# Performance work log

Measured on AMD Instinct MI355X. Metric: run time of the kernel, lower is better.

## Reference

```python
import jax, jax.numpy as jnp
import numpy as np

N_PTS = 1_000_000
RES = 512
RANK = 48
OUT = 32
INIT_SCALE = 0.1


def _plane_sample(plane, gx, gy):
    """Bilinear grid_sample, align_corners=True, border padding.
    plane: [R, Res, Res] (R=rank); gx, gy: [N] in [-1,1] -> [R, N]."""
    res = plane.shape[-1]
    px = jnp.clip((gx + 1.0) * 0.5 * (res - 1), 0.0, res - 1.0)
    py = jnp.clip((gy + 1.0) * 0.5 * (res - 1), 0.0, res - 1.0)
    x0 = jnp.floor(px).astype(jnp.int32)
    y0 = jnp.floor(py).astype(jnp.int32)
    x1 = jnp.minimum(x0 + 1, res - 1)
    y1 = jnp.minimum(y0 + 1, res - 1)
    wx = px - x0.astype(px.dtype)
    wy = py - y0.astype(py.dtype)
    # gathers: [R, N] each
    v00 = plane[:, y0, x0]
    v01 = plane[:, y0, x1]
    v10 = plane[:, y1, x0]
    v11 = plane[:, y1, x1]
    return (v00 * (1 - wy) * (1 - wx) + v01 * (1 - wy) * wx
            + v10 * wy * (1 - wx) + v11 * wy * wx)


def _line_sample(line, gy):
    """Line is [R, Res] (width dim of size 1 collapses; x coord is 0 -> px=0).
    1-D linear interp along Res with gy in [-1,1] -> [R, N]."""
    res = line.shape[-1]
    py = jnp.clip((gy + 1.0) * 0.5 * (res - 1), 0.0, res - 1.0)
    y0 = jnp.floor(py).astype(jnp.int32)
    y1 = jnp.minimum(y0 + 1, res - 1)
    wy = py - y0.astype(py.dtype)
    return line[:, y0] * (1 - wy) + line[:, y1] * wy


def _geo_forward(coordinates, plane_xy, plane_xz, plane_yz,
                 line_z, line_y, line_x, proj_w, proj_b):
    coords = coordinates * 2.0 - 1.0  # [N, 3] in [-1, 1]
    cx, cy, cz = coords[:, 0], coords[:, 1], coords[:, 2]
    vm = (_plane_sample(plane_xy, cx, cy) * _line_sample(line_z, cz)
          + _plane_sample(plane_xz, cx, cz) * _line_sample(line_y, cy)
          + _plane_sample(plane_yz, cy, cz) * _line_sample(line_x, cx))  # [R, N]
    # projection: [N, R] @ [R, OUT] + b
    return vm.T @ proj_w.T + proj_b


def setup_inputs() -> dict:
    key = jax.random.key(0)
    ks = jax.random.split(key, 9)
    return {
        "coordinates": jax.random.uniform(ks[0], (N_PTS, 3), dtype=jnp.float32),
        "plane_xy": jax.random.normal(ks[1], (RANK, RES, RES), jnp.float32) * INIT_SCALE,
        "plane_xz": jax.random.normal(ks[2], (RANK, RES, RES), jnp.float32) * INIT_SCALE,
        "plane_yz": jax.random.normal(ks[3], (RANK, RES, RES), jnp.float32) * INIT_SCALE,
        "line_z": jax.random.normal(ks[4], (RANK, RES), jnp.float32) * INIT_SCALE,
        "line_y": jax.random.normal(ks[5], (RANK, RES), jnp.float32) * INIT_SCALE,
        "line_x": jax.random.normal(ks[6], (RANK, RES), jnp.float32) * INIT_SCALE,
        "proj_w": jax.random.normal(ks[7], (OUT, RANK), jnp.float32) * INIT_SCALE,
        "proj_b": jnp.zeros((OUT,), jnp.float32),
    }


def reference(coordinates, plane_xy, plane_xz, plane_yz,
              line_z, line_y, line_x, proj_w, proj_b):
    return _geo_forward(coordinates, plane_xy, plane_xz, plane_yz,
                        line_z, line_y, line_x, proj_w, proj_b)
```

## Files before the change

### kernel.cpp

```cpp
#include <hip/hip_runtime.h>
#include <stdint.h>

#define RES      512
#define TEXELS   (RES * RES)
#define NPTS     1000000
#define RANK     48
#define ODIM     32
#define PPB      64
#define VMS      52
#define OSTR     36
#define TT       128
#define TS       25

typedef unsigned int u32;
typedef float vf4 __attribute__((ext_vector_type(4)));

__device__ __forceinline__ float lobf(u32 u) { return __uint_as_float(u << 16); }
__device__ __forceinline__ float hibf(u32 u) { return __uint_as_float(u & 0xffff0000u); }

__device__ __forceinline__ float ntl(const float* p) {
    return __builtin_nontemporal_load(p);
}

__device__ __forceinline__ u32 pkbf(float a, float b) {
    u32 x = __float_as_uint(a), y = __float_as_uint(b);
    u32 xr = (x + 0x7fffu + ((x >> 16) & 1u)) >> 16;
    u32 yr = (y + 0x7fffu + ((y >> 16) & 1u)) & 0xffff0000u;
    return xr | yr;
}

template <int TEXB>
__global__ __launch_bounds__(256) void transpose_planes(
    const float* __restrict__ p0, const float* __restrict__ p1,
    const float* __restrict__ p2, char* __restrict__ ws)
{
    __shared__ u32 lds[TT * TS + 8];

    int t = threadIdx.x;
    int base = blockIdx.x * TT;
    int plane = blockIdx.y;
    const float* src = (plane == 0) ? p0 : ((plane == 1) ? p1 : p2);

    int t7 = t & (TT - 1);
    int half = t >> 7;
#pragma unroll
    for (int j = 0; j < 12; ++j) {
        int d = half * 12 + j;
        float a = ntl(&src[(size_t)(2 * d) * TEXELS + base + t7]);
        float b = ntl(&src[(size_t)(2 * d + 1) * TEXELS + base + t7]);
        lds[t7 * TS + d] = pkbf(a, b);
    }
    __syncthreads();

    char* outp = ws + (size_t)plane * TEXELS * TEXB + (size_t)base * TEXB;
    constexpr int NS = TT * TEXB / (16 * 256);
#pragma unroll
    for (int s = 0; s < NS; ++s) {
        u32 o = (u32)(s * 256 + t) * 16u;
        u32 texel, rem;
        if (TEXB == 128) { texel = o >> 7; rem = o & 127u; }
        else {
            texel = ((o >> 5) * 43691u) >> 17;
            rem = o - texel * 96u;
        }
        u32 dw = texel * TS + (rem >> 2);
        uint4 q = make_uint4(lds[dw], lds[dw + 1], lds[dw + 2], lds[dw + 3]);
        *(uint4*)(outp + o) = q;
    }
}

template <int TEXB>
__global__ __launch_bounds__(256) void transpose_lines(
    const float* __restrict__ lz, const float* __restrict__ ly,
    const float* __restrict__ lx, char* __restrict__ ws)
{
    int id = blockIdx.x * 256 + threadIdx.x;
    int line = id >> 9;
    int pos = id & (RES - 1);
    const float* src = (line == 0) ? lz : ((line == 1) ? ly : lx);
    char* dst = ws + (size_t)3 * TEXELS * TEXB + (size_t)line * RES * TEXB
                   + (size_t)pos * TEXB;
#pragma unroll
    for (int k = 0; k < 6; ++k) {
        uint4 q;
        q.x = pkbf(ntl(&src[(8 * k + 0) * RES + pos]), ntl(&src[(8 * k + 1) * RES + pos]));
        q.y = pkbf(ntl(&src[(8 * k + 2) * RES + pos]), ntl(&src[(8 * k + 3) * RES + pos]));
        q.z = pkbf(ntl(&src[(8 * k + 4) * RES + pos]), ntl(&src[(8 * k + 5) * RES + pos]));
        q.w = pkbf(ntl(&src[(8 * k + 6) * RES + pos]), ntl(&src[(8 * k + 7) * RES + pos]));
        *(uint4*)(dst + 16 * k) = q;
    }
}

__device__ __forceinline__ void prep1(float g, int& i0, int& i1, float& w) {
    float p = fminf(fmaxf((g + 1.f) * 0.5f * 511.f, 0.f), 511.f);
    float fp = floorf(p);
    i0 = (int)fp;
    i1 = min(i0 + 1, RES - 1);
    w = p - fp;
}

template <int TEXB>
__global__ __launch_bounds__(512, 4) void geo_main(
    const float* __restrict__ coords, const char* __restrict__ ws,
    const float* __restrict__ W, const float* __restrict__ Bb,
    float* __restrict__ out)
{
    __shared__ float vm_lds[PPB * VMS];

    int tid = threadIdx.x;
    int ptL = tid >> 3;
    int c = tid & 7;
    int pt = blockIdx.x * PPB + ptL;

    float gx = ntl(&coords[3 * pt + 0]) * 2.f - 1.f;
    float gy = ntl(&coords[3 * pt + 1]) * 2.f - 1.f;
    float gz = ntl(&coords[3 * pt + 2]) * 2.f - 1.f;

    int x0, x1, y0, y1, z0, z1;
    float wx, wy, wz;
    prep1(gx, x0, x1, wx);
    prep1(gy, y0, y1, wy);
    prep1(gz, z0, z1, wz);

    const size_t PW = (size_t)TEXELS * TEXB;
    const size_t LW = (size_t)RES * TEXB;
    const char* pxy = ws;
    const char* pxz = ws + PW;
    const char* pyz = ws + 2 * PW;
    const char* lzb = ws + 3 * PW;
    const char* lyb = lzb + LW;
    const char* lxb = lyb + LW;

    u32 co = 12u * (u32)c;

    u32 q[12][3], le[3][3], lf[3][3];
    {
        u32 offs[12];
        offs[0] = (u32)(y0 * RES + x0) * TEXB + co;
        offs[1] = (u32)(y0 * RES + x1) * TEXB + co;
        offs[2] = (u32)(y1 * RES + x0) * TEXB + co;
        offs[3] = (u32)(y1 * RES + x1) * TEXB + co;
        offs[4] = (u32)(z0 * RES + x0) * TEXB + co;
        offs[5] = (u32)(z0 * RES + x1) * TEXB + co;
        offs[6] = (u32)(z1 * RES + x0) * TEXB + co;
        offs[7] = (u32)(z1 * RES + x1) * TEXB + co;
        offs[8]  = (u32)(z0 * RES + y0) * TEXB + co;
        offs[9]  = (u32)(z0 * RES + y1) * TEXB + co;
        offs[10] = (u32)(z1 * RES + y0) * TEXB + co;
        offs[11] = (u32)(z1 * RES + y1) * TEXB + co;
        const char* bases[3] = { pxy, pxz, pyz };
#pragma unroll
        for (int p = 0; p < 3; ++p) {
#pragma unroll
            for (int k = 0; k < 4; ++k) {
                const u32* s = (const u32*)(bases[p] + offs[4 * p + k]);
                q[4 * p + k][0] = s[0];
                q[4 * p + k][1] = s[1];
                q[4 * p + k][2] = s[2];
            }
        }
        const char* lb[3] = { lzb, lyb, lxb };
        u32 l0[3] = { (u32)z0 * TEXB + co, (u32)y0 * TEXB + co, (u32)x0 * TEXB + co };
        u32 l1[3] = { (u32)z1 * TEXB + co, (u32)y1 * TEXB + co, (u32)x1 * TEXB + co };
#pragma unroll
        for (int p = 0; p < 3; ++p) {
            const u32* s0 = (const u32*)(lb[p] + l0[p]);
            const u32* s1 = (const u32*)(lb[p] + l1[p]);
            le[p][0] = s0[0]; le[p][1] = s0[1]; le[p][2] = s0[2];
            lf[p][0] = s1[0]; lf[p][1] = s1[1]; lf[p][2] = s1[2];
        }
    }

    float pw[3][4];
    pw[0][0] = (1.f - wy) * (1.f - wx); pw[0][1] = (1.f - wy) * wx;
    pw[0][2] = wy * (1.f - wx);         pw[0][3] = wy * wx;
    pw[1][0] = (1.f - wz) * (1.f - wx); pw[1][1] = (1.f - wz) * wx;
    pw[1][2] = wz * (1.f - wx);         pw[1][3] = wz * wx;
    pw[2][0] = (1.f - wz) * (1.f - wy); pw[2][1] = (1.f - wz) * wy;
    pw[2][2] = wz * (1.f - wy);         pw[2][3] = wz * wy;
    float lw[3] = { wz, wy, wx };

    float vm[6] = { 0.f, 0.f, 0.f, 0.f, 0.f, 0.f };
#pragma unroll
    for (int p = 0; p < 3; ++p) {
        float s0 = pw[p][0], s1 = pw[p][1], s2 = pw[p][2], s3 = pw[p][3];
        float il = 1.f - lw[p], wl = lw[p];
#pragma unroll
        for (int d = 0; d < 3; ++d) {
            u32 a = q[4 * p + 0][d], b = q[4 * p + 1][d];
            u32 cc = q[4 * p + 2][d], dd = q[4 * p + 3][d];
            float slo = s0 * lobf(a) + s1 * lobf(b) + s2 * lobf(cc) + s3 * lobf(dd);
            float shi = s0 * hibf(a) + s1 * hibf(b) + s2 * hibf(cc) + s3 * hibf(dd);
            float llo = il * lobf(le[p][d]) + wl * lobf(lf[p][d]);
            float lhi = il * hibf(le[p][d]) + wl * hibf(lf[p][d]);
            vm[2 * d + 0] = fmaf(slo, llo, vm[2 * d + 0]);
            vm[2 * d + 1] = fmaf(shi, lhi, vm[2 * d + 1]);
        }
    }

    float* vr = vm_lds + ptL * VMS + 6 * c;
    *(float2*)(vr + 0) = make_float2(vm[0], vm[1]);
    *(float2*)(vr + 2) = make_float2(vm[2], vm[3]);
    *(float2*)(vr + 4) = make_float2(vm[4], vm[5]);

    __syncthreads();

    int wav = __builtin_amdgcn_readfirstlane(tid >> 6);
    int lane = tid & 63;
    int ob = wav * 4;

    const float* vmrow = vm_lds + lane * VMS;
    float4 bb = *(const float4*)(Bb + ob);
    float a0 = bb.x, a1 = bb.y, a2 = bb.z, a3 = bb.w;
#pragma unroll 4
    for (int k = 0; k < 12; ++k) {
        float4 v = *(const float4*)(vmrow + 4 * k);
        float4 w0 = *(const float4*)(W + (ob + 0) * RANK + 4 * k);
        float4 w1 = *(const float4*)(W + (ob + 1) * RANK + 4 * k);
        float4 w2 = *(const float4*)(W + (ob + 2) * RANK + 4 * k);
        float4 w3 = *(const float4*)(W + (ob + 3) * RANK + 4 * k);
        a0 = fmaf(v.x, w0.x, a0); a0 = fmaf(v.y, w0.y, a0);
        a0 = fmaf(v.z, w0.z, a0); a0 = fmaf(v.w, w0.w, a0);
        a1 = fmaf(v.x, w1.x, a1); a1 = fmaf(v.y, w1.y, a1);
        a1 = fmaf(v.z, w1.z, a1); a1 = fmaf(v.w, w1.w, a1);
        a2 = fmaf(v.x, w2.x, a2); a2 = fmaf(v.y, w2.y, a2);
        a2 = fmaf(v.z, w2.z, a2); a2 = fmaf(v.w, w2.w, a2);
        a3 = fmaf(v.x, w3.x, a3); a3 = fmaf(v.y, w3.y, a3);
        a3 = fmaf(v.z, w3.z, a3); a3 = fmaf(v.w, w3.w, a3);
    }

    __syncthreads();
    {
        vf4 r; r.x = a0; r.y = a1; r.z = a2; r.w = a3;
        *(vf4*)(vm_lds + lane * OSTR + ob) = r;
    }
    __syncthreads();
    {
        int p8 = lane >> 3;
        int c2 = lane & 7;
        vf4 v = *(const vf4*)(vm_lds + (wav * 8 + p8) * OSTR + 4 * c2);
        size_t o2 = (size_t)(blockIdx.x * PPB + wav * 8 + p8) * ODIM + 4 * c2;
        __builtin_nontemporal_store(v, (vf4*)(out + o2));
    }
}

template <int TEXB>
static void launch_all(const float* coords, const float* pxy, const float* pxz,
                       const float* pyz, const float* lz, const float* ly,
                       const float* lx, const float* W, const float* Bb,
                       float* out, char* ws, hipStream_t stream) {
    dim3 gt(TEXELS / TT, 3);
    transpose_planes<TEXB><<<gt, 256, 0, stream>>>(pxy, pxz, pyz, ws);
    transpose_lines<TEXB><<<6, 256, 0, stream>>>(lz, ly, lx, ws);
    geo_main<TEXB><<<NPTS / PPB, 512, 0, stream>>>(coords, ws, W, Bb, out);
}

extern "C" void kernel_launch(void* const* d_in, const int* in_sizes, int n_in,
                              void* d_out, int out_size, void* d_ws, size_t ws_size,
                              hipStream_t stream) {
    const float* coords = (const float*)d_in[0];
    const float* pxy = (const float*)d_in[1];
    const float* pxz = (const float*)d_in[2];
    const float* pyz = (const float*)d_in[3];
    const float* lz = (const float*)d_in[4];
    const float* ly = (const float*)d_in[5];
    const float* lx = (const float*)d_in[6];
    const float* W = (const float*)d_in[7];
    const float* Bb = (const float*)d_in[8];
    float* out = (float*)d_out;
    char* ws = (char*)d_ws;

    size_t need128 = (size_t)3 * TEXELS * 128 + (size_t)3 * RES * 128;
    if (ws_size >= need128)
        launch_all<128>(coords, pxy, pxz, pyz, lz, ly, lx, W, Bb, out, ws, stream);
    else
        launch_all<96>(coords, pxy, pxz, pyz, lz, ly, lx, W, Bb, out, ws, stream);
}
```

Before: 469.4 us.

## Sort points by Morton cell before sampling to improve gather locality

Adds a counting sort of points into 32^3 Morton-ordered cells (count, scan, scatter kernels) and runs the main sampling kernel on the reordered coordinates, scattering output rows back through a permutation. Block indices are also remapped so that consecutive sorted chunks land on the same XCD. The intent is to make the bilinear texel gathers from the 96-byte-per-texel planes cache-friendly instead of random. The cost is several extra kernel launches, global atomics on clustered cells, and an extra pass over the coordinates. The output LDS stride also changes from 36 to 33.

```diff
diff --git a/kernel.cpp b/kernel.cpp
--- a/kernel.cpp
+++ b/kernel.cpp
@@ -8,9 +8,10 @@
 #define ODIM     32
 #define PPB      64
 #define VMS      52
-#define OSTR     36
+#define OSTR     33
 #define TT       128
 #define TS       25
+#define CELLS    32768
 
 typedef unsigned int u32;
 typedef float vf4 __attribute__((ext_vector_type(4)));
@@ -19,6 +20,9 @@
 __device__ __forceinline__ float hibf(u32 u) { return __uint_as_float(u & 0xffff0000u); }
 
 __device__ __forceinline__ float ntl(const float* p) {
+    return __builtin_nontemporal_load(p);
+}
+__device__ __forceinline__ u32 ntlu(const u32* p) {
     return __builtin_nontemporal_load(p);
 }
 
@@ -27,6 +31,20 @@
     u32 xr = (x + 0x7fffu + ((x >> 16) & 1u)) >> 16;
     u32 yr = (y + 0x7fffu + ((y >> 16) & 1u)) & 0xffff0000u;
     return xr | yr;
+}
+
+__device__ __forceinline__ u32 sprd5(u32 a) {
+    a &= 31u;
+    a = (a | (a << 8)) & 0x100Fu;
+    a = (a | (a << 4)) & 0x10C3u;
+    a = (a | (a << 2)) & 0x1249u;
+    return a;
+}
+__device__ __forceinline__ u32 cellOf(float x, float y, float z) {
+    u32 cx = (u32)fminf(fmaxf(x * 32.f, 0.f), 31.f);
+    u32 cy = (u32)fminf(fmaxf(y * 32.f, 0.f), 31.f);
+    u32 cz = (u32)fminf(fmaxf(z * 32.f, 0.f), 31.f);
+    return sprd5(cx) | (sprd5(cy) << 1) | (sprd5(cz) << 2);
 }
 
 template <int TEXB>
@@ -91,6 +109,71 @@
     }
 }
 
+__global__ __launch_bounds__(256) void zero_counts(u32* __restrict__ counts) {
+    counts[blockIdx.x * 256 + threadIdx.x] = 0u;
+}
+
+__global__ __launch_bounds__(256) void cell_count(
+    const float* __restrict__ coords, u32* __restrict__ counts)
+{
+    int pt = blockIdx.x * 256 + threadIdx.x;
+    if (pt >= NPTS) return;
+    float x = ntl(&coords[3 * pt + 0]);
+    float y = ntl(&coords[3 * pt + 1]);
+    float z = ntl(&coords[3 * pt + 2]);
+    atomicAdd(&counts[cellOf(x, y, z)], 1u);
+}
+
+__global__ __launch_bounds__(1024) void cell_scan(
+    const u32* __restrict__ counts, u32* __restrict__ cursors)
+{
+    __shared__ u32 wt[16];
+    int t = threadIdx.x;
+    u32 local[32];
+    u32 s = 0;
+#pragma unroll
+    for (int i = 0; i < 32; ++i) {
+        local[i] = s;
+        s += counts[t * 32 + i];
+    }
+    u32 tot = s;
+    int lane = t & 63, w = t >> 6;
+    u32 incl = tot;
+#pragma unroll
+    for (int d = 1; d < 64; d <<= 1) {
+        u32 v = __shfl_up(incl, d);
+        if (lane >= d) incl += v;
+    }
+    if (lane == 63) wt[w] = incl;
+    __syncthreads();
+    if (t == 0) {
+        u32 a = 0;
+#pragma unroll
+        for (int i = 0; i < 16; ++i) { u32 x = wt[i]; wt[i] = a; a += x; }
+    }
+    __syncthreads();
+    u32 base = wt[w] + (incl - tot);
+#pragma unroll
+    for (int i = 0; i < 32; ++i)
+        cursors[t * 32 + i] = base + local[i];
+}
+
+__global__ __launch_bounds__(256) void cell_scatter(
+    const float* __restrict__ coords, u32* __restrict__ cursors,
+    u32* __restrict__ perm, float* __restrict__ rc)
+{
+    int pt = blockIdx.x * 256 + threadIdx.x;
+    if (pt >= NPTS) return;
+    float x = ntl(&coords[3 * pt + 0]);
+    float y = ntl(&coords[3 * pt + 1]);
+    float z = ntl(&coords[3 * pt + 2]);
+    u32 pos = atomicAdd(&cursors[cellOf(x, y, z)], 1u);
+    perm[pos] = (u32)pt;
+    rc[3 * pos + 0] = x;
+    rc[3 * pos + 1] = y;
+    rc[3 * pos + 2] = z;
+}
+
 __device__ __forceinline__ void prep1(float g, int& i0, int& i1, float& w) {
     float p = fminf(fmaxf((g + 1.f) * 0.5f * 511.f, 0.f), 511.f);
     float fp = floorf(p);
@@ -99,22 +182,35 @@
     w = p - fp;
 }
 
-template <int TEXB>
+template <int TEXB, bool SORTED>
 __global__ __launch_bounds__(512, 4) void geo_main(
     const float* __restrict__ coords, const char* __restrict__ ws,
+    const u32* __restrict__ perm,
     const float* __restrict__ W, const float* __restrict__ Bb,
     float* __restrict__ out)
 {
     __shared__ float vm_lds[PPB * VMS];
+    __shared__ u32 opt_lds[PPB];
 
     int tid = threadIdx.x;
     int ptL = tid >> 3;
     int c = tid & 7;
-    int pt = blockIdx.x * PPB + ptL;
+
+    int bid = blockIdx.x;
+    if (SORTED) {
+        int nwg = gridDim.x;
+        int q = nwg >> 3, r = nwg & 7;
+        int xcd = bid & 7, slot = bid >> 3;
+        bid = (xcd < r ? xcd * (q + 1) : r * (q + 1) + (xcd - r) * q) + slot;
+    }
+    int pt = bid * PPB + ptL;
 
     float gx = ntl(&coords[3 * pt + 0]) * 2.f - 1.f;
     float gy = ntl(&coords[3 * pt + 1]) * 2.f - 1.f;
     float gz = ntl(&coords[3 * pt + 2]) * 2.f - 1.f;
+
+    if (c == 0)
+        opt_lds[ptL] = SORTED ? ntlu(&perm[pt]) : (u32)pt;
 
     int x0, x1, y0, y1, z0, z1;
     float wx, wy, wz;
@@ -238,21 +334,22 @@
     {
         int p8 = lane >> 3;
         int c2 = lane & 7;
-        vf4 v = *(const vf4*)(vm_lds + (wav * 8 + p8) * OSTR + 4 * c2);
-        size_t o2 = (size_t)(blockIdx.x * PPB + wav * 8 + p8) * ODIM + 4 * c2;
-        __builtin_nontemporal_store(v, (vf4*)(out + o2));
+        int gp = wav * 8 + p8;
+        vf4 v = *(const vf4*)(vm_lds + gp * OSTR + 4 * c2);
+        size_t orow = (size_t)opt_lds[gp];
+        __builtin_nontemporal_store(v, (vf4*)(out + orow * ODIM + 4 * c2));
     }
 }
 
 template <int TEXB>
-static void launch_all(const float* coords, const float* pxy, const float* pxz,
-                       const float* pyz, const float* lz, const float* ly,
-                       const float* lx, const float* W, const float* Bb,
-                       float* out, char* ws, hipStream_t stream) {
+static void launch_unsorted(const float* coords, const float* pxy, const float* pxz,
+                            const float* pyz, const float* lz, const float* ly,
+                            const float* lx, const float* W, const float* Bb,
+                            float* out, char* ws, hipStream_t stream) {
     dim3 gt(TEXELS / TT, 3);
     transpose_planes<TEXB><<<gt, 256, 0, stream>>>(pxy, pxz, pyz, ws);
     transpose_lines<TEXB><<<6, 256, 0, stream>>>(lz, ly, lx, ws);
-    geo_main<TEXB><<<NPTS / PPB, 512, 0, stream>>>(coords, ws, W, Bb, out);
+    geo_main<TEXB, false><<<NPTS / PPB, 512, 0, stream>>>(coords, ws, nullptr, W, Bb, out);
 }
 
 extern "C" void kernel_launch(void* const* d_in, const int* in_sizes, int n_in,
@@ -270,9 +367,32 @@
     float* out = (float*)d_out;
     char* ws = (char*)d_ws;
 
+    size_t pool96 = (size_t)3 * TEXELS * 96 + (size_t)3 * RES * 96;
+    size_t o_counts = (pool96 + 255) & ~(size_t)255;
+    size_t o_cursors = o_counts + (size_t)CELLS * 4;
+    size_t o_perm = o_cursors + (size_t)CELLS * 4;
+    size_t o_rc = o_perm + (size_t)NPTS * 4;
+    size_t need_sorted = o_rc + (size_t)NPTS * 12;
     size_t need128 = (size_t)3 * TEXELS * 128 + (size_t)3 * RES * 128;
-    if (ws_size >= need128)
-        launch_all<128>(coords, pxy, pxz, pyz, lz, ly, lx, W, Bb, out, ws, stream);
-    else
-        launch_all<96>(coords, pxy, pxz, pyz, lz, ly, lx, W, Bb, out, ws, stream);
-}
+    size_t need96 = pool96;
+
+    if (ws_size >= need_sorted) {
+        u32* counts = (u32*)(ws + o_counts);
+        u32* cursors = (u32*)(ws + o_cursors);
+        u32* perm = (u32*)(ws + o_perm);
+        float* rc = (float*)(ws + o_rc);
+
+        dim3 gt(TEXELS / TT, 3);
+        transpose_planes<96><<<gt, 256, 0, stream>>>(pxy, pxz, pyz, ws);
+        transpose_lines<96><<<6, 256, 0, stream>>>(lz, ly, lx, ws);
+        zero_counts<<<CELLS / 256, 256, 0, stream>>>(counts);
+        cell_count<<<(NPTS + 255) / 256, 256, 0, stream>>>(coords, counts);
+        cell_scan<<<1, 1024, 0, stream>>>(counts, cursors);
+        cell_scatter<<<(NPTS + 255) / 256, 256, 0, stream>>>(coords, cursors, perm, rc);
+        geo_main<96, true><<<NPTS / PPB, 512, 0, stream>>>(rc, ws, perm, W, Bb, out);
+    } else if (ws_size >= need128) {
+        launch_unsorted<128>(coords, pxy, pxz, pyz, lz, ly, lx, W, Bb, out, ws, stream);
+    } else {
+        launch_unsorted<96>(coords, pxy, pxz, pyz, lz, ly, lx, W, Bb, out, ws, stream);
+    }
+}
```

After: 483.3 us. 1.03x slower.

## Spatially bin points by Morton cell before sampling to improve gather locality

Applied to the files above, without the earlier changes.

Adds a three-kernel counting sort (per-segment histogram, scan, scatter) that groups points into 4096 Morton-ordered cells and stores sorted coordinates with their original index. The main kernel then reads the sorted points, remaps block IDs so each XCD handles a contiguous range, and scatters its outputs back to the original rows. The goal is better cache locality for the random plane gathers, paid for with extra passes over the coordinates, atomics, and scattered output writes. It also vectorises the plane transpose loads, changes the output LDS stride, and forces the 96-byte texel layout on the sorted path.

```diff
diff --git a/kernel.cpp b/kernel.cpp
--- a/kernel.cpp
+++ b/kernel.cpp
@@ -8,9 +8,13 @@
 #define ODIM     32
 #define PPB      64
 #define VMS      52
-#define OSTR     36
+#define OSTR     33
 #define TT       128
 #define TS       25
+#define NCELL    4096
+#define NB       32
+#define SEG      31250
+#define ENTR     (NCELL * NB)
 
 typedef unsigned int u32;
 typedef float vf4 __attribute__((ext_vector_type(4)));
@@ -20,6 +24,9 @@
 
 __device__ __forceinline__ float ntl(const float* p) {
     return __builtin_nontemporal_load(p);
+}
+__device__ __forceinline__ vf4 ntl4(const float* p) {
+    return __builtin_nontemporal_load((const vf4*)p);
 }
 
 __device__ __forceinline__ u32 pkbf(float a, float b) {
@@ -29,29 +36,41 @@
     return xr | yr;
 }
 
+__device__ __forceinline__ u32 sprd4(u32 a) {
+    a &= 15u;
+    a = (a | (a << 4)) & 0x0C3u;
+    a = (a | (a << 2)) & 0x249u;
+    return a;
+}
+__device__ __forceinline__ u32 cellOf(float x, float y, float z) {
+    u32 cx = (u32)fminf(fmaxf(x * 16.f, 0.f), 15.f);
+    u32 cy = (u32)fminf(fmaxf(y * 16.f, 0.f), 15.f);
+    u32 cz = (u32)fminf(fmaxf(z * 16.f, 0.f), 15.f);
+    return sprd4(cx) | (sprd4(cy) << 1) | (sprd4(cz) << 2);
+}
+
 template <int TEXB>
 __global__ __launch_bounds__(256) void transpose_planes(
     const float* __restrict__ p0, const float* __restrict__ p1,
     const float* __restrict__ p2, char* __restrict__ ws)
 {
     __shared__ u32 lds[TT * TS + 8];
-
     int t = threadIdx.x;
     int base = blockIdx.x * TT;
     int plane = blockIdx.y;
     const float* src = (plane == 0) ? p0 : ((plane == 1) ? p1 : p2);
-
-    int t7 = t & (TT - 1);
-    int half = t >> 7;
-#pragma unroll
-    for (int j = 0; j < 12; ++j) {
-        int d = half * 12 + j;
-        float a = ntl(&src[(size_t)(2 * d) * TEXELS + base + t7]);
-        float b = ntl(&src[(size_t)(2 * d + 1) * TEXELS + base + t7]);
-        lds[t7 * TS + d] = pkbf(a, b);
-    }
-    __syncthreads();
-
+    int xi = t & 31, dg = t >> 5;
+#pragma unroll
+    for (int j = 0; j < 3; ++j) {
+        int d = dg + 8 * j;
+        vf4 a = ntl4(src + (size_t)(2 * d) * TEXELS + base + 4 * xi);
+        vf4 b = ntl4(src + (size_t)(2 * d + 1) * TEXELS + base + 4 * xi);
+        lds[(4 * xi + 0) * TS + d] = pkbf(a.x, b.x);
+        lds[(4 * xi + 1) * TS + d] = pkbf(a.y, b.y);
+        lds[(4 * xi + 2) * TS + d] = pkbf(a.z, b.z);
+        lds[(4 * xi + 3) * TS + d] = pkbf(a.w, b.w);
+    }
+    __syncthreads();
     char* outp = ws + (size_t)plane * TEXELS * TEXB + (size_t)base * TEXB;
     constexpr int NS = TT * TEXB / (16 * 256);
 #pragma unroll
@@ -59,10 +78,7 @@
         u32 o = (u32)(s * 256 + t) * 16u;
         u32 texel, rem;
         if (TEXB == 128) { texel = o >> 7; rem = o & 127u; }
-        else {
-            texel = ((o >> 5) * 43691u) >> 17;
-            rem = o - texel * 96u;
-        }
+        else { texel = ((o >> 5) * 43691u) >> 17; rem = o - texel * 96u; }
         u32 dw = texel * TS + (rem >> 2);
         uint4 q = make_uint4(lds[dw], lds[dw + 1], lds[dw + 2], lds[dw + 3]);
         *(uint4*)(outp + o) = q;
@@ -91,6 +107,87 @@
     }
 }
 
+__global__ __launch_bounds__(1024) void bin_count(
+    const float* __restrict__ coords, u32* __restrict__ T)
+{
+    __shared__ u32 hist[NCELL];
+    int blk = blockIdx.x, t = threadIdx.x;
+#pragma unroll
+    for (int i = 0; i < NCELL / 1024; ++i) hist[t + 1024 * i] = 0u;
+    __syncthreads();
+    int lim = (blk + 1) * SEG;
+#pragma unroll 1
+    for (int it = 0; it < (SEG + 1023) / 1024; ++it) {
+        int idx = blk * SEG + it * 1024 + t;
+        if (idx < lim) {
+            float x = ntl(&coords[3 * idx + 0]);
+            float y = ntl(&coords[3 * idx + 1]);
+            float z = ntl(&coords[3 * idx + 2]);
+            atomicAdd(&hist[cellOf(x, y, z)], 1u);
+        }
+    }
+    __syncthreads();
+#pragma unroll
+    for (int i = 0; i < NCELL / 1024; ++i) {
+        int cell = t + 1024 * i;
+        T[(u32)cell * NB + blk] = hist[cell];
+    }
+}
+
+__global__ __launch_bounds__(1024) void bin_scan(
+    const u32* __restrict__ T, u32* __restrict__ C)
+{
+    __shared__ u32 wt[16];
+    int t = threadIdx.x;
+    const int PER = ENTR / 1024;
+    const u32* tp = T + t * PER;
+    u32 tot = 0;
+#pragma unroll 16
+    for (int i = 0; i < PER; ++i) tot += tp[i];
+    int lane = t & 63, w = t >> 6;
+    u32 incl = tot;
+#pragma unroll
+    for (int d = 1; d < 64; d <<= 1) {
+        u32 v = __shfl_up(incl, d);
+        if (lane >= d) incl += v;
+    }
+    if (lane == 63) wt[w] = incl;
+    __syncthreads();
+    u32 run = incl - tot;
+#pragma unroll
+    for (int i = 0; i < 16; ++i) run += (i < w) ? wt[i] : 0u;
+    u32* op = C + t * PER;
+#pragma unroll 16
+    for (int i = 0; i < PER; ++i) { u32 v = tp[i]; op[i] = run; run += v; }
+}
+
+__global__ __launch_bounds__(1024) void bin_scatter(
+    const float* __restrict__ coords, const u32* __restrict__ C,
+    vf4* __restrict__ rc2)
+{
+    __shared__ u32 cur[NCELL];
+    int blk = blockIdx.x, t = threadIdx.x;
+#pragma unroll
+    for (int i = 0; i < NCELL / 1024; ++i) {
+        int cell = t + 1024 * i;
+        cur[cell] = C[(u32)cell * NB + blk];
+    }
+    __syncthreads();
+    int lim = (blk + 1) * SEG;
+#pragma unroll 1
+    for (int it = 0; it < (SEG + 1023) / 1024; ++it) {
+        int idx = blk * SEG + it * 1024 + t;
+        if (idx < lim) {
+            float x = ntl(&coords[3 * idx + 0]);
+            float y = ntl(&coords[3 * idx + 1]);
+            float z = ntl(&coords[3 * idx + 2]);
+            u32 pos = atomicAdd(&cur[cellOf(x, y, z)], 1u);
+            vf4 v; v.x = x; v.y = y; v.z = z; v.w = __uint_as_float((u32)idx);
+            __builtin_nontemporal_store(v, rc2 + pos);
+        }
+    }
+}
+
 __device__ __forceinline__ void prep1(float g, int& i0, int& i1, float& w) {
     float p = fminf(fmaxf((g + 1.f) * 0.5f * 511.f, 0.f), 511.f);
     float fp = floorf(p);
@@ -99,22 +196,42 @@
     w = p - fp;
 }
 
-template <int TEXB>
+template <int TEXB, bool SORTED>
 __global__ __launch_bounds__(512, 4) void geo_main(
-    const float* __restrict__ coords, const char* __restrict__ ws,
+    const void* __restrict__ cin, const char* __restrict__ ws,
     const float* __restrict__ W, const float* __restrict__ Bb,
     float* __restrict__ out)
 {
     __shared__ float vm_lds[PPB * VMS];
+    __shared__ u32 opt_lds[PPB];
 
     int tid = threadIdx.x;
     int ptL = tid >> 3;
     int c = tid & 7;
-    int pt = blockIdx.x * PPB + ptL;
-
-    float gx = ntl(&coords[3 * pt + 0]) * 2.f - 1.f;
-    float gy = ntl(&coords[3 * pt + 1]) * 2.f - 1.f;
-    float gz = ntl(&coords[3 * pt + 2]) * 2.f - 1.f;
+
+    int bid = blockIdx.x;
+    if (SORTED) {
+        int nwg = gridDim.x;
+        int q = nwg >> 3, r = nwg & 7;
+        int xcd = bid & 7, slot = bid >> 3;
+        bid = (xcd < r ? xcd * (q + 1) : r * (q + 1) + (xcd - r) * q) + slot;
+    }
+    int pt = bid * PPB + ptL;
+
+    float gx, gy, gz;
+    if (SORTED) {
+        vf4 cc = __builtin_nontemporal_load((const vf4*)cin + pt);
+        gx = cc.x * 2.f - 1.f;
+        gy = cc.y * 2.f - 1.f;
+        gz = cc.z * 2.f - 1.f;
+        if (c == 0) opt_lds[ptL] = __float_as_uint(cc.w);
+    } else {
+        const float* coords = (const float*)cin;
+        gx = ntl(&coords[3 * pt + 0]) * 2.f - 1.f;
+        gy = ntl(&coords[3 * pt + 1]) * 2.f - 1.f;
+        gz = ntl(&coords[3 * pt + 2]) * 2.f - 1.f;
+        if (c == 0) opt_lds[ptL] = (u32)pt;
+    }
 
     int x0, x1, y0, y1, z0, z1;
     float wx, wy, wz;
@@ -238,21 +355,22 @@
     {
         int p8 = lane >> 3;
         int c2 = lane & 7;
-        vf4 v = *(const vf4*)(vm_lds + (wav * 8 + p8) * OSTR + 4 * c2);
-        size_t o2 = (size_t)(blockIdx.x * PPB + wav * 8 + p8) * ODIM + 4 * c2;
-        __builtin_nontemporal_store(v, (vf4*)(out + o2));
+        int gp = wav * 8 + p8;
+        vf4 v = *(const vf4*)(vm_lds + gp * OSTR + 4 * c2);
+        size_t orow = (size_t)opt_lds[gp];
+        __builtin_nontemporal_store(v, (vf4*)(out + orow * ODIM + 4 * c2));
     }
 }
 
 template <int TEXB>
-static void launch_all(const float* coords, const float* pxy, const float* pxz,
-                       const float* pyz, const float* lz, const float* ly,
-                       const float* lx, const float* W, const float* Bb,
-                       float* out, char* ws, hipStream_t stream) {
+static void launch_unsorted(const float* coords, const float* pxy, const float* pxz,
+                            const float* pyz, const float* lz, const float* ly,
+                            const float* lx, const float* W, const float* Bb,
+                            float* out, char* ws, hipStream_t stream) {
     dim3 gt(TEXELS / TT, 3);
     transpose_planes<TEXB><<<gt, 256, 0, stream>>>(pxy, pxz, pyz, ws);
     transpose_lines<TEXB><<<6, 256, 0, stream>>>(lz, ly, lx, ws);
-    geo_main<TEXB><<<NPTS / PPB, 512, 0, stream>>>(coords, ws, W, Bb, out);
+    geo_main<TEXB, false><<<NPTS / PPB, 512, 0, stream>>>(coords, ws, W, Bb, out);
 }
 
 extern "C" void kernel_launch(void* const* d_in, const int* in_sizes, int n_in,
@@ -270,9 +388,28 @@
     float* out = (float*)d_out;
     char* ws = (char*)d_ws;
 
+    size_t pool96 = (size_t)3 * TEXELS * 96 + (size_t)3 * RES * 96;
+    size_t o_T = (pool96 + 255) & ~(size_t)255;
+    size_t o_C = o_T + (size_t)ENTR * 4;
+    size_t o_rc2 = o_C + (size_t)ENTR * 4;
+    size_t need_sorted = o_rc2 + (size_t)NPTS * 16;
     size_t need128 = (size_t)3 * TEXELS * 128 + (size_t)3 * RES * 128;
-    if (ws_size >= need128)
-        launch_all<128>(coords, pxy, pxz, pyz, lz, ly, lx, W, Bb, out, ws, stream);
-    else
-        launch_all<96>(coords, pxy, pxz, pyz, lz, ly, lx, W, Bb, out, ws, stream);
-}
+
+    if (ws_size >= need_sorted) {
+        u32* T = (u32*)(ws + o_T);
+        u32* C = (u32*)(ws + o_C);
+        vf4* rc2 = (vf4*)(ws + o_rc2);
+
+        dim3 gt(TEXELS / TT, 3);
+        transpose_planes<96><<<gt, 256, 0, stream>>>(pxy, pxz, pyz, ws);
+        transpose_lines<96><<<6, 256, 0, stream>>>(lz, ly, lx, ws);
+        bin_count<<<NB, 1024, 0, stream>>>(coords, T);
+        bin_scan<<<1, 1024, 0, stream>>>(T, C);
+        bin_scatter<<<NB, 1024, 0, stream>>>(coords, C, rc2);
+        geo_main<96, true><<<NPTS / PPB, 512, 0, stream>>>(rc2, ws, W, Bb, out);
+    } else if (ws_size >= need128) {
+        launch_unsorted<128>(coords, pxy, pxz, pyz, lz, ly, lx, W, Bb, out, ws, stream);
+    } else {
+        launch_unsorted<96>(coords, pxy, pxz, pyz, lz, ly, lx, W, Bb, out, ws, stream);
+    }
+}
```

Measured after the change: 493.7 us. 1.05x slower.
